# Performance work log

Measured on AMD Instinct MI355X. Metric: run time of the kernel, lower is better.

Reference implementation:

```python
import jax, jax.numpy as jnp
import numpy as np

B, L, D, H, F = 4, 1024, 512, 8, 2048
HD = D // H  # head_dim used only for the concat/reshape trick
INF = 1e9


def layer_norm(x, g, b, eps=1e-6):
    mu = jnp.mean(x, -1, keepdims=True)
    var = jnp.mean((x - mu) ** 2, -1, keepdims=True)
    return (x - mu) / jnp.sqrt(var + eps) * g + b


def setup_inputs() -> dict:
    key = jax.random.key(0)
    ks = jax.random.split(key, 16)
    s = 0.02
    tokens = jax.random.normal(ks[0], (B, L, D), jnp.float32)
    inp_lens = jax.random.randint(ks[1], (B,), 1, L + 1)
    # causal mask: 1 where attention is disallowed (added as mask * -1e9)
    self_mask = jnp.triu(jnp.ones((L, L), jnp.float32), 1)
    # self-attention per-head full-D projections (nn.Linear weight convention [out,in])
    wq = jax.random.normal(ks[2], (H, D, D), jnp.float32) * s
    wk = jax.random.normal(ks[3], (H, D, D), jnp.float32) * s
    wv = jax.random.normal(ks[4], (H, D, D), jnp.float32) * s
    wo = jax.random.normal(ks[5], (D, H * D), jnp.float32) * s  # Linear(H*D -> D)
    # FFN
    w1 = jax.random.normal(ks[6], (F, D), jnp.float32) * s
    b1 = jnp.zeros((F,), jnp.float32)
    w2 = jax.random.normal(ks[7], (D, F), jnp.float32) * s
    b2 = jnp.zeros((D,), jnp.float32)
    # cross-attention per-head full-D projections
    cwk = jax.random.normal(ks[8], (H, D, D), jnp.float32) * s
    cwv = jax.random.normal(ks[9], (H, D, D), jnp.float32) * s
    cwq = jax.random.normal(ks[10], (H, D, D), jnp.float32) * s
    ln1_g = jnp.ones((D,), jnp.float32); ln1_b = jnp.zeros((D,), jnp.float32)
    ln2_g = jnp.ones((D,), jnp.float32); ln2_b = jnp.zeros((D,), jnp.float32)
    return dict(tokens=tokens, inp_lens=inp_lens, self_mask=self_mask,
                ln1_g=ln1_g, ln1_b=ln1_b, ln2_g=ln2_g, ln2_b=ln2_b,
                wq=wq, wk=wk, wv=wv, wo=wo, w1=w1, b1=b1, w2=w2, b2=b2,
                cwk=cwk, cwv=cwv, cwq=cwq)


def reference(tokens, inp_lens, self_mask, ln1_g, ln1_b, ln2_g, ln2_b,
              wq, wk, wv, wo, w1, b1, w2, b2, cwk, cwv, cwq):
    scale = 1.0 / jnp.sqrt(jnp.float32(D))
    # --- pre-norm + multi-head self attention (each head full-D QKV) ---
    x = layer_norm(tokens, ln1_g, ln1_b)
    q = jnp.einsum('bld,hod->bhlo', x, wq)
    k = jnp.einsum('bld,hod->bhlo', x, wk)
    v = jnp.einsum('bld,hod->bhlo', x, wv)
    logits = jnp.einsum('bhld,bhmd->bhlm', q, k) * scale + self_mask * (-INF)
    self_W = jax.nn.softmax(logits, axis=-1)            # [B,H,L,L]
    ctx = jnp.einsum('bhlm,bhmd->bhld', self_W, v)       # [B,H,L,D]
    # replicate torch concat/view: ctx[h].view(B,L,H,hd), cat over heads, flatten
    comb = ctx.reshape(B, H, L, H, HD).transpose(0, 2, 3, 1, 4).reshape(B, L, H * D)
    sa = jnp.einsum('blk,dk->bld', comb, wo)
    t = tokens + sa
    # --- FFN block ---
    y = layer_norm(t, ln2_g, ln2_b)
    h1 = jax.nn.gelu(jnp.einsum('bld,fd->blf', y, w1) + b1, approximate=False)
    t = t + (jnp.einsum('blf,df->bld', h1, w2) + b2)
    # --- cross attention: K/V from ORIGINAL tokens, Q from post-FFN tokens ---
    # (apply_mask=cross_mask=None -> no mask; context is computed but discarded upstream)
    ck = jnp.einsum('bld,hod->bhlo', tokens, cwk)
    cq = jnp.einsum('bld,hod->bhlo', t, cwq)
    clogits = jnp.einsum('bhld,bhmd->bhlm', cq, ck) * scale
    cross_W = jax.nn.softmax(clogits, axis=-1)           # [B,H,L,L]
    return (t, self_W, cross_W)
```

## Files before the change

### kernel.cpp

```cpp
#include <hip/hip_runtime.h>
#include <hip/hip_bf16.h>


typedef __attribute__((ext_vector_type(4))) float f32x4;
typedef __attribute__((ext_vector_type(8))) short bf16x8;

#define SCALE 0.04419417382415922f

__device__ __forceinline__ short f2bf(float f) {
  __hip_bfloat16 h = __float2bfloat16(f);
  short s; __builtin_memcpy(&s, &h, 2); return s;
}
__device__ __forceinline__ float bf2f(short s) {
  unsigned int u = ((unsigned int)(unsigned short)s) << 16;
  float f; __builtin_memcpy(&f, &u, 4); return f;
}

__device__ __forceinline__ void gload16(const void* g, void* lds) {
  __builtin_amdgcn_global_load_lds(
      (const __attribute__((address_space(1))) unsigned int*)g,
      (__attribute__((address_space(3))) unsigned int*)lds, 16, 0, 0);
}

__device__ __forceinline__ float block_sum(float v, float* sm) {
  #pragma unroll
  for (int o = 1; o < 64; o <<= 1) v += __shfl_xor(v, o, 64);
  int w = threadIdx.x >> 6;
  if ((threadIdx.x & 63) == 0) sm[w] = v;
  __syncthreads();
  float r = sm[0] + sm[1] + sm[2] + sm[3];
  __syncthreads();
  return r;
}

__global__ __launch_bounds__(256) void prep(
    const float* __restrict__ tokens, const float* __restrict__ ln1g,
    const float* __restrict__ ln1b,
    const float* __restrict__ w1, const float* __restrict__ w2,
    const float* __restrict__ wo,
    const float* __restrict__ wq, const float* __restrict__ wk,
    const float* __restrict__ cwq, const float* __restrict__ cwk,
    const float* __restrict__ wv,
    short* __restrict__ xb, short* __restrict__ tokb,
    short* __restrict__ w1b, short* __restrict__ w2b,
    short* __restrict__ wop, short* __restrict__ QT, short* __restrict__ KT,
    short* __restrict__ WVT) {
  __shared__ float sm[4];
  __shared__ float tile[32][33];
  const int bid = blockIdx.x;
  if (bid < 4096) {
    size_t row = bid;
    const float2 v = reinterpret_cast<const float2*>(tokens + row * 512)[threadIdx.x];
    short2 ro; ro.x = f2bf(v.x); ro.y = f2bf(v.y);
    reinterpret_cast<short2*>(tokb + row * 512)[threadIdx.x] = ro;
    float mu = block_sum(v.x + v.y, sm) * (1.0f / 512.0f);
    float dx = v.x - mu, dy = v.y - mu;
    float var = block_sum(dx * dx + dy * dy, sm) * (1.0f / 512.0f);
    float rs = rsqrtf(var + 1e-6f);
    int c = threadIdx.x * 2;
    short2 o;
    o.x = f2bf(dx * rs * ln1g[c] + ln1b[c]);
    o.y = f2bf(dy * rs * ln1g[c + 1] + ln1b[c + 1]);
    reinterpret_cast<short2*>(xb + row * 512)[threadIdx.x] = o;
  } else if (bid < 6144) {
    int i = (bid - 4096) * 256 + threadIdx.x;
    const float* src; short* dst; int k;
    if (i < 262144) { src = w1; dst = w1b; k = i; }
    else            { src = w2; dst = w2b; k = i - 262144; }
    float4 v = reinterpret_cast<const float4*>(src)[k];
    short4 o; o.x = f2bf(v.x); o.y = f2bf(v.y); o.z = f2bf(v.z); o.w = f2bf(v.w);
    reinterpret_cast<short4*>(dst)[k] = o;
  } else if (bid < 14336) {
    int i = (bid - 6144) * 256 + threadIdx.x;
    int o = i >> 12, j = i & 4095;
    int h = j >> 9, d = j & 511;
    int h2 = d >> 6, e = d & 63;
    wop[i] = f2bf(wo[(o << 12) + h2 * 512 + h * 64 + e]);
  } else {
    const int idx = bid - 14336;
    const int z = idx >> 8, t = z >> 3, h = z & 7;
    const int tl = idx & 255, by = tl >> 4, bx = tl & 15;
    const float* in = (t == 0) ? wq : (t == 1) ? wk : (t == 2) ? cwq
                    : (t == 3) ? cwk : wv;
    short* out = (t == 0) ? QT : (t == 1) ? KT
               : (t == 2) ? (QT + 2097152) : (t == 3) ? (KT + 2097152) : WVT;
    const int tx = threadIdx.x & 31, ty = threadIdx.x >> 5;
    const size_t base = (size_t)h * 262144;
    #pragma unroll
    for (int r = 0; r < 4; ++r) {
      const int o = by * 32 + ty + r * 8;
      tile[ty + r * 8][tx] = in[base + (size_t)o * 512 + bx * 32 + tx];
    }
    __syncthreads();
    #pragma unroll
    for (int r = 0; r < 4; ++r) {
      const int d = bx * 32 + ty + r * 8;
      out[base + (size_t)d * 512 + by * 32 + tx] = f2bf(tile[tx][ty + r * 8]);
    }
  }
}

__global__ __launch_bounds__(256) void ln2_fuse(
    const float* __restrict__ tokens,
    const float* __restrict__ p0, const float* __restrict__ p1,
    const float* __restrict__ gw, const float* __restrict__ bw,
    float* __restrict__ tf, short* __restrict__ yb) {
  __shared__ float sm[4];
  size_t row = blockIdx.x;
  const size_t i2 = row * 256 + threadIdx.x;
  const float2 tv = reinterpret_cast<const float2*>(tokens)[i2];
  const float2 a2 = reinterpret_cast<const float2*>(p0)[i2];
  const float2 b2 = reinterpret_cast<const float2*>(p1)[i2];
  float x0 = tv.x + a2.x + b2.x, x1 = tv.y + a2.y + b2.y;
  float2 o2; o2.x = x0; o2.y = x1;
  reinterpret_cast<float2*>(tf)[i2] = o2;
  float mu = block_sum(x0 + x1, sm) * (1.0f / 512.0f);
  float dx = x0 - mu, dy = x1 - mu;
  float var = block_sum(dx * dx + dy * dy, sm) * (1.0f / 512.0f);
  float rs = rsqrtf(var + 1e-6f);
  int c = threadIdx.x * 2;
  short2 o;
  o.x = f2bf(dx * rs * gw[c] + bw[c]);
  o.y = f2bf(dy * rs * gw[c + 1] + bw[c + 1]);
  reinterpret_cast<short2*>(yb + row * 512)[threadIdx.x] = o;
}

template<int CAUSAL>
__global__ __launch_bounds__(256) void rownorm(const short* __restrict__ E,
    float* __restrict__ W, short* __restrict__ pout) {
  const int wv = threadIdx.x >> 6, l = threadIdx.x & 63;
  const size_t row = (size_t)blockIdx.x * 4 + wv;
  const int r = (int)(row & 1023);
  const int live_end = CAUSAL ? (((r >> 7) + 1) << 7) : 1024;
  const short* ep = E + row * 1024;
  float s = 0.f;
  #pragma unroll
  for (int c = 0; c < 2; ++c) {
    const int c0 = c * 512 + l * 8;
    if (c0 < live_end) {
      bf16x8 v = *reinterpret_cast<const bf16x8*>(ep + c0);
      #pragma unroll
      for (int j = 0; j < 8; ++j) s += bf2f(v[j]);
    }
  }
  #pragma unroll
  for (int o = 1; o < 64; o <<= 1) s += __shfl_xor(s, o, 64);
  const float inv = 1.0f / s;
  float* wp = W + row * 1024;
  #pragma unroll
  for (int c = 0; c < 4; ++c) {
    const int c0 = c * 256 + l * 4;
    float4 o4;
    if (c0 < live_end) {
      short4 v = *reinterpret_cast<const short4*>(ep + c0);
      o4.x = bf2f(v.x) * inv; o4.y = bf2f(v.y) * inv;
      o4.z = bf2f(v.z) * inv; o4.w = bf2f(v.w) * inv;
      if (CAUSAL)
        *reinterpret_cast<short4*>(pout + row * 1024 + c0) =
            make_short4(f2bf(o4.x), f2bf(o4.y), f2bf(o4.z), f2bf(o4.w));
    } else { o4.x = o4.y = o4.z = o4.w = 0.f; }
    *reinterpret_cast<float4*>(wp + c0) = o4;
  }
}

template<int EPI, int BN>
__global__ __launch_bounds__(256, 2) void gemm_nt(
    const short* __restrict__ A, const short* __restrict__ Bw,
    int K, const float* __restrict__ fin, const float* __restrict__ fin2,
    float* __restrict__ fout, short* __restrict__ bout,
    short* __restrict__ bout2,
    const short* __restrict__ A3, const short* __restrict__ B3) {
  constexpr int NJ = BN / 32;
  __shared__ short As[128 * 64];
  __shared__ short Bs[BN * 64];
  const int tid = threadIdx.x;
  const int w = tid >> 6, l = tid & 63;
  const int wr = w >> 1, wc = w & 1;
  const int lr = l & 15, kh = l >> 4;
  const int sx = lr & 7;
  int bx = blockIdx.x, by = blockIdx.y;
  const int z = blockIdx.z;
  if constexpr (EPI == 1) {
    int idx = blockIdx.x;
    by = (int)((sqrtf(8.0f * idx + 1.0f) - 1.0f) * 0.5f);
    while ((by + 1) * (by + 2) / 2 <= idx) ++by;
    while (by * (by + 1) / 2 > idx) --by;
    bx = idx - by * (by + 1) / 2;
  }
  const int bm = by * 128, bn = bx * BN;
  const int ar = w * 8 + (l >> 3);
  const int ac = ((l & 7) ^ (ar & 7)) << 3;
  const short* Ab = A; const short* Bb = Bw;
  int lda = K;
  if constexpr (EPI == 1 || EPI == 7) {
    Ab = A + (size_t)z * 524288;
    Bb = Bw + (size_t)(z >> 3) * 524288;
  } else if constexpr (EPI == 8) {
    const int zz = blockIdx.z;
    if (zz < 16) { Ab = A + (size_t)zz * 262144; Bb = Bw + (size_t)zz * 262144; }
    else { Ab = A3 + (size_t)(zz - 16) * 512; Bb = B3 + (size_t)(zz - 16) * 262144;
           lda = 4096; }
  }

  f32x4 acc[4][NJ];
  #pragma unroll
  for (int i = 0; i < 4; ++i)
    #pragma unroll
    for (int j = 0; j < NJ; ++j) acc[i][j] = (f32x4){0.f, 0.f, 0.f, 0.f};

  for (int k0 = 0; k0 < K; k0 += 64) {
    #pragma unroll
    for (int c = 0; c < 4; ++c)
      gload16(Ab + (size_t)(bm + c * 32 + ar) * lda + k0 + ac, &As[c * 2048 + w * 512]);
    #pragma unroll
    for (int c = 0; c < BN / 32; ++c)
      gload16(Bb + (size_t)(bn + c * 32 + ar) * K + k0 + ac, &Bs[c * 2048 + w * 512]);
    __syncthreads();
    bf16x8 af[4][2], bfr[NJ][2];
    #pragma unroll
    for (int i = 0; i < 4; ++i) {
      const int row_ = wr * 64 + i * 16 + lr;
      #pragma unroll
      for (int ks = 0; ks < 2; ++ks)
        af[i][ks] = *reinterpret_cast<const bf16x8*>(
            &As[row_ * 64 + ((((ks << 2) + kh) ^ sx) << 3)]);
    }
    #pragma unroll
    for (int j = 0; j < NJ; ++j) {
      const int row_ = wc * (BN / 2) + j * 16 + lr;
      #pragma unroll
      for (int ks = 0; ks < 2; ++ks)
        bfr[j][ks] = *reinterpret_cast<const bf16x8*>(
            &Bs[row_ * 64 + ((((ks << 2) + kh) ^ sx) << 3)]);
    }
    #pragma unroll
    for (int i = 0; i < 4; ++i)
      #pragma unroll
      for (int j = 0; j < NJ; ++j)
        #pragma unroll
        for (int ks = 0; ks < 2; ++ks)
          acc[i][j] = __builtin_amdgcn_mfma_f32_16x16x32_bf16(
              bfr[j][ks], af[i][ks], acc[i][j], 0, 0, 0);
    __syncthreads();
  }

  #pragma unroll
  for (int i = 0; i < 4; ++i) {
    const int grow = bm + wr * 64 + i * 16 + lr;
    #pragma unroll
    for (int j = 0; j < NJ; ++j) {
      const int gcol0 = bn + wc * (BN / 2) + j * 16 + kh * 4;
      const float v0 = acc[i][j][0], v1 = acc[i][j][1];
      const float v2 = acc[i][j][2], v3 = acc[i][j][3];
      if constexpr (EPI == 0) {
        const int b = grow >> 10, lw = grow & 1023;
        if (bn < 4096) {
          const int h = gcol0 >> 9, o = gcol0 & 511;
          *reinterpret_cast<short4*>(&bout[(((size_t)(b * 8 + h)) * 1024 + lw) * 512 + o]) =
              make_short4(f2bf(v0), f2bf(v1), f2bf(v2), f2bf(v3));
        } else {
          const int n2 = gcol0 - 4096, h = n2 >> 9, o = n2 & 511;
          const size_t base = ((size_t)(b * 8 + h)) * 512;
          bout2[(base + o + 0) * 1024 + lw] = f2bf(v0);
          bout2[(base + o + 1) * 1024 + lw] = f2bf(v1);
          bout2[(base + o + 2) * 1024 + lw] = f2bf(v2);
          bout2[(base + o + 3) * 1024 + lw] = f2bf(v3);
        }
      } else if constexpr (EPI == 1) {
        short4 o;
        o.x = (gcol0 + 0 > grow) ? (short)0 : f2bf(__expf(v0 * SCALE - 8.0f));
        o.y = (gcol0 + 1 > grow) ? (short)0 : f2bf(__expf(v1 * SCALE - 8.0f));
        o.z = (gcol0 + 2 > grow) ? (short)0 : f2bf(__expf(v2 * SCALE - 8.0f));
        o.w = (gcol0 + 3 > grow) ? (short)0 : f2bf(__expf(v3 * SCALE - 8.0f));
        *reinterpret_cast<short4*>(&bout[(size_t)z * 1048576 + (size_t)grow * 1024 + gcol0]) = o;
      } else if constexpr (EPI == 4) {
        const float4 b4 = *reinterpret_cast<const float4*>(&fin[gcol0]);
        const float x0 = v0 + b4.x, x1 = v1 + b4.y, x2 = v2 + b4.z, x3 = v3 + b4.w;
        const float g0 = 0.5f * x0 * (1.0f + erff(x0 * 0.70710678118654752f));
        const float g1 = 0.5f * x1 * (1.0f + erff(x1 * 0.70710678118654752f));
        const float g2 = 0.5f * x2 * (1.0f + erff(x2 * 0.70710678118654752f));
        const float g3 = 0.5f * x3 * (1.0f + erff(x3 * 0.70710678118654752f));
        *reinterpret_cast<short4*>(&bout[(size_t)grow * 2048 + gcol0]) =
            make_short4(f2bf(g0), f2bf(g1), f2bf(g2), f2bf(g3));
      } else if constexpr (EPI == 5) {
        const size_t idx = (size_t)grow * 512 + gcol0;
        const float4 a4 = *reinterpret_cast<const float4*>(&fin2[idx]);
        const float4 b4 = *reinterpret_cast<const float4*>(&fin[gcol0]);
        float4 f;
        f.x = a4.x + v0 + b4.x; f.y = a4.y + v1 + b4.y;
        f.z = a4.z + v2 + b4.z; f.w = a4.w + v3 + b4.w;
        *reinterpret_cast<float4*>(&fout[idx]) = f;
        *reinterpret_cast<short4*>(&bout[idx]) =
            make_short4(f2bf(f.x), f2bf(f.y), f2bf(f.z), f2bf(f.w));
      } else if constexpr (EPI == 6) {
        const int b = grow >> 10, lw = grow & 1023;
        const int h = gcol0 >> 9, o = gcol0 & 511;
        *reinterpret_cast<short4*>(&bout[(((size_t)(b * 8 + h)) * 1024 + lw) * 512 + o]) =
            make_short4(f2bf(v0), f2bf(v1), f2bf(v2), f2bf(v3));
      } else if constexpr (EPI == 7) {
        short4 o;
        o.x = f2bf(__expf(v0 * SCALE - 8.0f));
        o.y = f2bf(__expf(v1 * SCALE - 8.0f));
        o.z = f2bf(__expf(v2 * SCALE - 8.0f));
        o.w = f2bf(__expf(v3 * SCALE - 8.0f));
        *reinterpret_cast<short4*>(&bout[(size_t)z * 1048576 + (size_t)grow * 1024 + gcol0]) = o;
      } else if constexpr (EPI == 8) {
        const int zz = blockIdx.z;
        short* outp = (zz < 8)  ? (bout + (size_t)zz * 262144)
                    : (zz < 16) ? (bout2 + (size_t)(zz - 8) * 262144)
                                : (bout + 2097152 + (size_t)(zz - 16) * 262144);
        *reinterpret_cast<short4*>(&outp[(size_t)grow * 512 + gcol0]) =
            make_short4(f2bf(v0), f2bf(v1), f2bf(v2), f2bf(v3));
      }
    }
  }
}

__global__ __launch_bounds__(256, 2) void pv_sa(
    const short* __restrict__ P, const short* __restrict__ uT,
    float* __restrict__ part) {
  __shared__ short As[128 * 64];
  __shared__ short Bs[64 * 64];
  const int tid = threadIdx.x;
  const int w = tid >> 6, l = tid & 63;
  const int wr = w >> 1, wc = w & 1;
  const int lr = l & 15, kh = l >> 4;
  const int sx = lr & 7;
  const int bn = blockIdx.x * 64;
  const int bm = blockIdx.y * 128;
  const int b = blockIdx.z >> 1, half = blockIdx.z & 1;
  const int ar = w * 8 + (l >> 3);
  const int ac = ((l & 7) ^ (ar & 7)) << 3;
  const int kend = bm + 128;

  f32x4 acc[4][2];
  #pragma unroll
  for (int i = 0; i < 4; ++i)
    #pragma unroll
    for (int j = 0; j < 2; ++j) acc[i][j] = (f32x4){0.f, 0.f, 0.f, 0.f};

  for (int h = half * 4; h < half * 4 + 4; ++h) {
    const short* Ab = P + ((size_t)(b * 8 + h) << 20);
    const short* Bb = uT + (size_t)(b * 8 + h) * 524288;
    for (int k0 = 0; k0 < kend; k0 += 64) {
      #pragma unroll
      for (int c = 0; c < 4; ++c)
        gload16(Ab + (size_t)(bm + c * 32 + ar) * 1024 + k0 + ac, &As[c * 2048 + w * 512]);
      #pragma unroll
      for (int c = 0; c < 2; ++c)
        gload16(Bb + (size_t)(bn + c * 32 + ar) * 1024 + k0 + ac, &Bs[c * 2048 + w * 512]);
      __syncthreads();
      bf16x8 af[4][2], bfr[2][2];
      #pragma unroll
      for (int i = 0; i < 4; ++i) {
        const int row_ = wr * 64 + i * 16 + lr;
        #pragma unroll
        for (int ks = 0; ks < 2; ++ks)
          af[i][ks] = *reinterpret_cast<const bf16x8*>(
              &As[row_ * 64 + ((((ks << 2) + kh) ^ sx) << 3)]);
      }
      #pragma unroll
      for (int j = 0; j < 2; ++j) {
        const int row_ = wc * 32 + j * 16 + lr;
        #pragma unroll
        for (int ks = 0; ks < 2; ++ks)
          bfr[j][ks] = *reinterpret_cast<const bf16x8*>(
              &Bs[row_ * 64 + ((((ks << 2) + kh) ^ sx) << 3)]);
      }
      #pragma unroll
      for (int i = 0; i < 4; ++i)
        #pragma unroll
        for (int j = 0; j < 2; ++j)
          #pragma unroll
          for (int ks = 0; ks < 2; ++ks)
            acc[i][j] = __builtin_amdgcn_mfma_f32_16x16x32_bf16(
                bfr[j][ks], af[i][ks], acc[i][j], 0, 0, 0);
      __syncthreads();
    }
  }

  float* plane = part + (size_t)half * 2097152;
  #pragma unroll
  for (int i = 0; i < 4; ++i) {
    const int grow = bm + wr * 64 + i * 16 + lr;
    #pragma unroll
    for (int j = 0; j < 2; ++j) {
      const int gcol0 = bn + wc * 32 + j * 16 + kh * 4;
      float4 f;
      f.x = acc[i][j][0]; f.y = acc[i][j][1];
      f.z = acc[i][j][2]; f.w = acc[i][j][3];
      *reinterpret_cast<float4*>(&plane[((size_t)(b * 1024 + grow)) * 512 + gcol0]) = f;
    }
  }
}

extern "C" void kernel_launch(void* const* d_in, const int* in_sizes, int n_in,
                              void* d_out, int out_size, void* d_ws, size_t ws_size,
                              hipStream_t stream) {
  const float* tokens = (const float*)d_in[0];
  const float* ln1g = (const float*)d_in[3];
  const float* ln1b = (const float*)d_in[4];
  const float* ln2g = (const float*)d_in[5];
  const float* ln2b = (const float*)d_in[6];
  const float* wq = (const float*)d_in[7];
  const float* wk = (const float*)d_in[8];
  const float* wv = (const float*)d_in[9];
  const float* wo = (const float*)d_in[10];
  const float* w1 = (const float*)d_in[11];
  const float* b1 = (const float*)d_in[12];
  const float* w2 = (const float*)d_in[13];
  const float* b2 = (const float*)d_in[14];
  const float* cwk = (const float*)d_in[15];
  const float* cwq = (const float*)d_in[17];

  float* out_t = (float*)d_out;
  float* out_self = out_t + 2097152;
  float* out_cross = out_self + 33554432;

  char* ws = (char*)d_ws;
  size_t off = 0;
  auto alloc = [&](size_t bytes) -> void* {
    void* p = ws + off; off = (off + bytes + 255) & ~(size_t)255; return p;
  };
  short* xb   = (short*)alloc(2097152ull * 2);
  short* tokb = (short*)alloc(2097152ull * 2);
  float* tf   = (float*)alloc(2097152ull * 4);
  short* tb   = (short*)alloc(2097152ull * 2);
  short* yb   = (short*)alloc(2097152ull * 2);
  short* h1b  = (short*)alloc(8388608ull * 2);
  short* qb   = (short*)alloc(16777216ull * 2);
  short* utb  = (short*)alloc(16777216ull * 2);
  short* Eb   = (short*)alloc(33554432ull * 2);
  float* pvp  = (float*)alloc(4194304ull * 4);
  short* Wstk = (short*)alloc(4194304ull * 2);
  short* Mstk = (short*)alloc(2097152ull * 2);
  short* wop  = (short*)alloc(2097152ull * 2);
  short* w1b  = (short*)alloc(1048576ull * 2);
  short* w2b  = (short*)alloc(1048576ull * 2);
  short* QT   = (short*)alloc(4194304ull * 2);
  short* KT   = (short*)alloc(4194304ull * 2);
  short* WVT  = (short*)alloc(2097152ull * 2);

  prep<<<24576, 256, 0, stream>>>(tokens, ln1g, ln1b, w1, w2, wo,
                                  wq, wk, cwq, cwk, wv,
                                  xb, tokb, w1b, w2b, wop, QT, KT, WVT);
  gemm_nt<8, 128><<<dim3(4, 4, 24), 256, 0, stream>>>(KT, QT, 512,
      nullptr, nullptr, nullptr, Wstk, Mstk, wop, WVT);
  gemm_nt<0, 128><<<dim3(64, 32, 1), 256, 0, stream>>>(xb, Wstk, 512,
      nullptr, nullptr, nullptr, qb, utb, nullptr, nullptr);
  gemm_nt<1, 128><<<dim3(36, 1, 32), 256, 0, stream>>>(qb, xb, 512,
      nullptr, nullptr, nullptr, Eb, nullptr, nullptr, nullptr);
  rownorm<1><<<8192, 256, 0, stream>>>(Eb, out_self, Eb);
  pv_sa<<<dim3(8, 8, 8), 256, 0, stream>>>(Eb, utb, pvp);
  ln2_fuse<<<4096, 256, 0, stream>>>(tokens, pvp, pvp + 2097152,
                                     ln2g, ln2b, tf, yb);
  gemm_nt<4, 128><<<dim3(16, 32, 1), 256, 0, stream>>>(yb, w1b, 512,
      b1, nullptr, nullptr, h1b, nullptr, nullptr, nullptr);
  gemm_nt<5, 64><<<dim3(8, 32, 1), 256, 0, stream>>>(h1b, w2b, 2048,
      b2, tf, out_t, tb, nullptr, nullptr, nullptr);
  gemm_nt<6, 128><<<dim3(32, 32, 1), 256, 0, stream>>>(tb, Mstk, 512,
      nullptr, nullptr, nullptr, qb, nullptr, tb, Mstk);
  gemm_nt<7, 128><<<dim3(8, 8, 32), 256, 0, stream>>>(qb, tokb, 512,
      nullptr, nullptr, nullptr, Eb, nullptr, nullptr, nullptr);
  rownorm<0><<<8192, 256, 0, stream>>>(Eb, out_cross, nullptr);
}
```

Baseline: 420.8 us.

## Double-buffer LDS tiles in gemm_nt and pv_sa to overlap loads with MFMA

Both the generic GEMM kernel and the P·V kernel now keep two LDS buffers. The next K-tile is prefetched with global_load_lds while MFMAs run on the current tile, and each step ends with one barrier instead of two. The pv_sa loop is flattened across heads so the prefetch also spans head boundaries, and s_setprio raises wave priority around the MFMA block. LDS use doubles, which may lower occupancy below the two blocks per CU that the launch bounds target. Because the next tile is issued before the current tile's LDS reads, correctness depends on the explicit waitcnt and barrier placement.

```diff
diff --git a/kernel.cpp b/kernel.cpp
--- a/kernel.cpp
+++ b/kernel.cpp
@@ -171,8 +171,8 @@
     short* __restrict__ bout2,
     const short* __restrict__ A3, const short* __restrict__ B3) {
   constexpr int NJ = BN / 32;
-  __shared__ short As[128 * 64];
-  __shared__ short Bs[BN * 64];
+  __shared__ short As[2][128 * 64];
+  __shared__ short Bs[2][BN * 64];
   const int tid = threadIdx.x;
   const int w = tid >> 6, l = tid & 63;
   const int wr = w >> 1, wc = w & 1;
@@ -202,20 +202,33 @@
            lda = 4096; }
   }
 
+  auto stage = [&](int sbuf, int kc) {
+    #pragma unroll
+    for (int c = 0; c < 4; ++c)
+      gload16(Ab + (size_t)(bm + c * 32 + ar) * lda + kc + ac,
+              &As[sbuf][c * 2048 + w * 512]);
+    #pragma unroll
+    for (int c = 0; c < BN / 32; ++c)
+      gload16(Bb + (size_t)(bn + c * 32 + ar) * K + kc + ac,
+              &Bs[sbuf][c * 2048 + w * 512]);
+  };
+
   f32x4 acc[4][NJ];
   #pragma unroll
   for (int i = 0; i < 4; ++i)
     #pragma unroll
     for (int j = 0; j < NJ; ++j) acc[i][j] = (f32x4){0.f, 0.f, 0.f, 0.f};
 
+  stage(0, 0);
+  asm volatile("s_waitcnt vmcnt(0)" ::: "memory");
+  __builtin_amdgcn_s_barrier();
+
+  int cur = 0;
   for (int k0 = 0; k0 < K; k0 += 64) {
-    #pragma unroll
-    for (int c = 0; c < 4; ++c)
-      gload16(Ab + (size_t)(bm + c * 32 + ar) * lda + k0 + ac, &As[c * 2048 + w * 512]);
-    #pragma unroll
-    for (int c = 0; c < BN / 32; ++c)
-      gload16(Bb + (size_t)(bn + c * 32 + ar) * K + k0 + ac, &Bs[c * 2048 + w * 512]);
-    __syncthreads();
+    const bool more = (k0 + 64 < K);
+    if (more) stage(cur ^ 1, k0 + 64);
+    const short* Ac = As[cur];
+    const short* Bc = Bs[cur];
     bf16x8 af[4][2], bfr[NJ][2];
     #pragma unroll
     for (int i = 0; i < 4; ++i) {
@@ -223,7 +236,7 @@
       #pragma unroll
       for (int ks = 0; ks < 2; ++ks)
         af[i][ks] = *reinterpret_cast<const bf16x8*>(
-            &As[row_ * 64 + ((((ks << 2) + kh) ^ sx) << 3)]);
+            &Ac[row_ * 64 + ((((ks << 2) + kh) ^ sx) << 3)]);
     }
     #pragma unroll
     for (int j = 0; j < NJ; ++j) {
@@ -231,8 +244,11 @@
       #pragma unroll
       for (int ks = 0; ks < 2; ++ks)
         bfr[j][ks] = *reinterpret_cast<const bf16x8*>(
-            &Bs[row_ * 64 + ((((ks << 2) + kh) ^ sx) << 3)]);
-    }
+            &Bc[row_ * 64 + ((((ks << 2) + kh) ^ sx) << 3)]);
+    }
+    asm volatile("s_waitcnt lgkmcnt(0)" ::: "memory");
+    __builtin_amdgcn_sched_barrier(0);
+    __builtin_amdgcn_s_setprio(1);
     #pragma unroll
     for (int i = 0; i < 4; ++i)
       #pragma unroll
@@ -241,7 +257,12 @@
         for (int ks = 0; ks < 2; ++ks)
           acc[i][j] = __builtin_amdgcn_mfma_f32_16x16x32_bf16(
               bfr[j][ks], af[i][ks], acc[i][j], 0, 0, 0);
-    __syncthreads();
+    __builtin_amdgcn_s_setprio(0);
+    if (more) {
+      asm volatile("s_waitcnt vmcnt(0)" ::: "memory");
+      __builtin_amdgcn_s_barrier();
+      cur ^= 1;
+    }
   }
 
   #pragma unroll
@@ -319,8 +340,8 @@
 __global__ __launch_bounds__(256, 2) void pv_sa(
     const short* __restrict__ P, const short* __restrict__ uT,
     float* __restrict__ part) {
-  __shared__ short As[128 * 64];
-  __shared__ short Bs[64 * 64];
+  __shared__ short As[2][128 * 64];
+  __shared__ short Bs[2][64 * 64];
   const int tid = threadIdx.x;
   const int w = tid >> 6, l = tid & 63;
   const int wr = w >> 1, wc = w & 1;
@@ -332,6 +353,20 @@
   const int ar = w * 8 + (l >> 3);
   const int ac = ((l & 7) ^ (ar & 7)) << 3;
   const int kend = bm + 128;
+  const int hend = half * 4 + 4;
+
+  auto stage = [&](int sbuf, int hh, int kc) {
+    const short* Ah = P + ((size_t)(b * 8 + hh) << 20);
+    const short* Bh = uT + (size_t)(b * 8 + hh) * 524288;
+    #pragma unroll
+    for (int c = 0; c < 4; ++c)
+      gload16(Ah + (size_t)(bm + c * 32 + ar) * 1024 + kc + ac,
+              &As[sbuf][c * 2048 + w * 512]);
+    #pragma unroll
+    for (int c = 0; c < 2; ++c)
+      gload16(Bh + (size_t)(bn + c * 32 + ar) * 1024 + kc + ac,
+              &Bs[sbuf][c * 2048 + w * 512]);
+  };
 
   f32x4 acc[4][2];
   #pragma unroll
@@ -339,44 +374,51 @@
     #pragma unroll
     for (int j = 0; j < 2; ++j) acc[i][j] = (f32x4){0.f, 0.f, 0.f, 0.f};
 
-  for (int h = half * 4; h < half * 4 + 4; ++h) {
-    const short* Ab = P + ((size_t)(b * 8 + h) << 20);
-    const short* Bb = uT + (size_t)(b * 8 + h) * 524288;
-    for (int k0 = 0; k0 < kend; k0 += 64) {
-      #pragma unroll
-      for (int c = 0; c < 4; ++c)
-        gload16(Ab + (size_t)(bm + c * 32 + ar) * 1024 + k0 + ac, &As[c * 2048 + w * 512]);
-      #pragma unroll
-      for (int c = 0; c < 2; ++c)
-        gload16(Bb + (size_t)(bn + c * 32 + ar) * 1024 + k0 + ac, &Bs[c * 2048 + w * 512]);
-      __syncthreads();
-      bf16x8 af[4][2], bfr[2][2];
-      #pragma unroll
-      for (int i = 0; i < 4; ++i) {
-        const int row_ = wr * 64 + i * 16 + lr;
+  int h = half * 4, k0 = 0, cur = 0;
+  stage(0, h, 0);
+  asm volatile("s_waitcnt vmcnt(0)" ::: "memory");
+  __builtin_amdgcn_s_barrier();
+
+  while (true) {
+    int nh = h, nk = k0 + 64;
+    bool more = true;
+    if (nk >= kend) { nh = h + 1; nk = 0; more = (nh < hend); }
+    if (more) stage(cur ^ 1, nh, nk);
+    const short* Ac = As[cur];
+    const short* Bc = Bs[cur];
+    bf16x8 af[4][2], bfr[2][2];
+    #pragma unroll
+    for (int i = 0; i < 4; ++i) {
+      const int row_ = wr * 64 + i * 16 + lr;
+      #pragma unroll
+      for (int ks = 0; ks < 2; ++ks)
+        af[i][ks] = *reinterpret_cast<const bf16x8*>(
+            &Ac[row_ * 64 + ((((ks << 2) + kh) ^ sx) << 3)]);
+    }
+    #pragma unroll
+    for (int j = 0; j < 2; ++j) {
+      const int row_ = wc * 32 + j * 16 + lr;
+      #pragma unroll
+      for (int ks = 0; ks < 2; ++ks)
+        bfr[j][ks] = *reinterpret_cast<const bf16x8*>(
+            &Bc[row_ * 64 + ((((ks << 2) + kh) ^ sx) << 3)]);
+    }
+    asm volatile("s_waitcnt lgkmcnt(0)" ::: "memory");
+    __builtin_amdgcn_sched_barrier(0);
+    __builtin_amdgcn_s_setprio(1);
+    #pragma unroll
+    for (int i = 0; i < 4; ++i)
+      #pragma unroll
+      for (int j = 0; j < 2; ++j)
         #pragma unroll
         for (int ks = 0; ks < 2; ++ks)
-          af[i][ks] = *reinterpret_cast<const bf16x8*>(
-              &As[row_ * 64 + ((((ks << 2) + kh) ^ sx) << 3)]);
-      }
-      #pragma unroll
-      for (int j = 0; j < 2; ++j) {
-        const int row_ = wc * 32 + j * 16 + lr;
-        #pragma unroll
-        for (int ks = 0; ks < 2; ++ks)
-          bfr[j][ks] = *reinterpret_cast<const bf16x8*>(
-              &Bs[row_ * 64 + ((((ks << 2) + kh) ^ sx) << 3)]);
-      }
-      #pragma unroll
-      for (int i = 0; i < 4; ++i)
-        #pragma unroll
-        for (int j = 0; j < 2; ++j)
-          #pragma unroll
-          for (int ks = 0; ks < 2; ++ks)
-            acc[i][j] = __builtin_amdgcn_mfma_f32_16x16x32_bf16(
-                bfr[j][ks], af[i][ks], acc[i][j], 0, 0, 0);
-      __syncthreads();
-    }
+          acc[i][j] = __builtin_amdgcn_mfma_f32_16x16x32_bf16(
+              bfr[j][ks], af[i][ks], acc[i][j], 0, 0, 0);
+    __builtin_amdgcn_s_setprio(0);
+    if (!more) break;
+    asm volatile("s_waitcnt vmcnt(0)" ::: "memory");
+    __builtin_amdgcn_s_barrier();
+    cur ^= 1; h = nh; k0 = nk;
   }
 
   float* plane = part + (size_t)half * 2097152;
```

Measured after the change: 458.5 us. +9.0%, slower.
